# Kernel optimization log

Hardware: AMD Instinct MI355X
Metric: run time of the kernel (lower is better)

The kernel has to match this reference:

```python
import jax, jax.numpy as jnp
from jax import lax
import numpy as np


def setup_inputs() -> dict:
    key = jax.random.key(0)
    ks = jax.random.split(key, 9)
    B, T, F, E, H, O = 64, 512, 64, 256, 512, 128
    s = lambda k, shape, fan: jax.random.normal(k, shape, jnp.float32) / np.sqrt(fan)
    return {
        "x": jax.random.normal(ks[0], (B, T, F), jnp.float32),
        "W_emb": s(ks[1], (E, F), F),
        "b_emb": jnp.zeros((E,), jnp.float32),
        "W_ih": s(ks[2], (4 * H, E), E),
        "W_hh": s(ks[3], (4 * H, H), H),
        "b_ih": jnp.zeros((4 * H,), jnp.float32),
        "b_hh": jnp.zeros((4 * H,), jnp.float32),
        "W_fc": s(ks[4], (O, H), H),
        "b_fc": jnp.zeros((O,), jnp.float32),
    }


def reference(x, W_emb, b_emb, W_ih, W_hh, b_ih, b_hh, W_fc, b_fc):
    # Linear embedding: [B,T,F] -> [B,T,E]
    e = jnp.einsum("btf,ef->bte", x, W_emb) + b_emb
    # Precompute input-side gate projections once (big GEMM): [B,T,4H]
    xg = jnp.einsum("bte,ge->btg", e, W_ih) + b_ih + b_hh
    B = x.shape[0]
    H = W_hh.shape[1]
    W_hh_T = W_hh.T  # [H,4H]

    def step(carry, xt):
        h, c = carry
        gates = xt + h @ W_hh_T  # [B,4H]
        i, f, g, o = jnp.split(gates, 4, axis=-1)  # PyTorch LSTM gate order
        i = jax.nn.sigmoid(i)
        f = jax.nn.sigmoid(f)
        g = jnp.tanh(g)
        o = jax.nn.sigmoid(o)
        c = f * c + i * g
        h = o * jnp.tanh(c)
        return (h, c), h

    h0 = jnp.zeros((B, H), x.dtype)
    _, hs = lax.scan(step, (h0, h0), jnp.swapaxes(xg, 0, 1))  # hs: [T,B,H]
    # AdaptiveAvgPool1d(1) over time -> mean over T
    pooled = hs.mean(axis=0)  # [B,H]
    return pooled @ W_fc.T + b_fc  # [B,O]
```

## Files before the change

### kernel.cpp

```cpp
#include <hip/hip_runtime.h>
#include <math.h>

#define TS 512
#define NB 64
#define NF 64
#define NE 256
#define NH 512
#define NO 128

#define NGRP 4
#define NSLC 32
#define RPG  16

#define OFF_WCOMB 0
#define OFF_BCOMB 131072
#define OFF_HBUF  133120
#define OFF_POOL  198656

typedef short bf16x8 __attribute__((ext_vector_type(8)));
typedef float f32x4 __attribute__((ext_vector_type(4)));
typedef unsigned long long u64;
typedef unsigned int u32;

union F8 { bf16x8 s; unsigned short u[8]; };

__device__ __forceinline__ unsigned short f2bf(float f) {
    unsigned u = __float_as_uint(f);
    u += 0x7fffu + ((u >> 16) & 1u);
    return (unsigned short)(u >> 16);
}
__device__ __forceinline__ float bf2f(unsigned short h) {
    return __uint_as_float(((unsigned)h) << 16);
}
__device__ __forceinline__ float fast_sigmoid(float v) {
    return 1.f / (1.f + __expf(-v));
}
__device__ __forceinline__ float fast_tanh(float v) {
    return 1.f - 2.f / (1.f + __expf(2.f * v));
}
__device__ __forceinline__ u32 aload(const u32* p) {
    return __hip_atomic_load(p, __ATOMIC_RELAXED, __HIP_MEMORY_SCOPE_AGENT);
}

__global__ __launch_bounds__(256) void k_wcomb(const float* __restrict__ W_emb,
                                               const float* __restrict__ b_emb,
                                               const float* __restrict__ W_ih,
                                               const float* __restrict__ b_ih,
                                               const float* __restrict__ b_hh,
                                               float* __restrict__ W_comb,
                                               float* __restrict__ b_comb) {
    __shared__ float wih[4][NE];
    int g0 = blockIdx.x * 4;
    for (int i = threadIdx.x; i < 4 * NE; i += 256)
        wih[i >> 8][i & 255] = W_ih[(size_t)g0 * NE + i];
    __syncthreads();
    int gl = threadIdx.x >> 6, f = threadIdx.x & 63;
    float acc = 0.f;
    for (int e = 0; e < NE; ++e) acc += wih[gl][e] * W_emb[e * NF + f];
    W_comb[(size_t)(g0 + gl) * NF + f] = acc;
    if (f == 0) {
        float a2 = 0.f;
        for (int e = 0; e < NE; ++e) a2 += wih[gl][e] * b_emb[e];
        b_comb[g0 + gl] = a2 + b_ih[g0 + gl] + b_hh[g0 + gl];
    }
}

__global__ __launch_bounds__(512, 1) void k_lstm(const float* __restrict__ x,
                                                 const float* __restrict__ W_hh,
                                                 const float* __restrict__ W_comb,
                                                 const float* __restrict__ b_comb,
                                                 u32* __restrict__ hbuf,
                                                 float* __restrict__ pooled) {
    const int wg = blockIdx.x;
    const int grp = wg & 3;
    const int slc = wg >> 2;
    const int tid = threadIdx.x;
    const int lane = tid & 63, wave = tid >> 6;
    const int m4 = lane & 15;
    const int qq = lane >> 4;

    const int mtn = (wave < 6) ? 2 : 3;
    int kts[3];
    kts[0] = (wave < 6) ? 2 * wave : 12 + 2 * (wave - 6);
    kts[1] = kts[0] + 1;
    kts[2] = (wave < 6) ? 0 : 16 + (wave - 6);

    __shared__ __align__(16) float part[8 * 64 * 20];
    __shared__ float bcl[64];

    F8 bhi[4][3], blo[4][3];
    #pragma unroll
    for (int nt = 0; nt < 4; ++nt) {
        const int grow = nt * NH + slc * 16 + m4;
        #pragma unroll
        for (int k = 0; k < 3; ++k) {
            if (k < mtn) {
                const int kt = kts[k];
                const float* wp = (kt < 16)
                    ? W_hh   + (size_t)grow * NH + kt * 32 + qq * 8
                    : W_comb + (size_t)grow * NF + (kt - 16) * 32 + qq * 8;
                const float4 w0 = *(const float4*)wp;
                const float4 w1 = *(const float4*)(wp + 4);
                float wf[8] = {w0.x, w0.y, w0.z, w0.w, w1.x, w1.y, w1.z, w1.w};
                #pragma unroll
                for (int e = 0; e < 8; ++e) {
                    unsigned short hb = f2bf(wf[e]);
                    bhi[nt][k].u[e] = hb;
                    blo[nt][k].u[e] = f2bf(wf[e] - bf2f(hb));
                }
            }
        }
    }

    if (tid < 64) bcl[tid] = b_comb[(tid >> 4) * NH + slc * 16 + (tid & 15)];

    F8 ahi[3], alo[3];
    #pragma unroll
    for (int k = 0; k < 3; ++k) {
        ahi[k].s = (bf16x8){0, 0, 0, 0, 0, 0, 0, 0};
        alo[k].s = (bf16x8){0, 0, 0, 0, 0, 0, 0, 0};
    }
    float4 xpa = make_float4(0.f, 0.f, 0.f, 0.f), xpb = xpa;
    if (wave >= 6) {
        const int xoff = (wave - 6) * 32 + qq * 8;
        const float* xr0 = x + ((size_t)(grp * RPG + m4) * TS + 0) * NF + xoff;
        const float4 a = ((const float4*)xr0)[0];
        const float4 b4 = ((const float4*)xr0)[1];
        float xf[8] = {a.x, a.y, a.z, a.w, b4.x, b4.y, b4.z, b4.w};
        #pragma unroll
        for (int e = 0; e < 8; ++e) {
            unsigned short hb = f2bf(xf[e]);
            ahi[2].u[e] = hb;
            alo[2].u[e] = f2bf(xf[e] - bf2f(hb));
        }
        const float* xr1 = x + ((size_t)(grp * RPG + m4) * TS + 1) * NF + xoff;
        xpa = ((const float4*)xr1)[0];
        xpb = ((const float4*)xr1)[1];
    }

    float c_reg = 0.f, hsum = 0.f;
    __syncthreads();

    for (int t = 0; t < TS; ++t) {
        const bool last = (t + 1 == TS);
        const int p = t & 1;

        f32x4 acc[4][3];
        #pragma unroll
        for (int nt = 0; nt < 4; ++nt)
            #pragma unroll
            for (int c = 0; c < 3; ++c) acc[nt][c] = (f32x4){0.f, 0.f, 0.f, 0.f};
        #pragma unroll
        for (int k = 0; k < 3; ++k) {
            if (k < mtn) {
                const bf16x8 ah = ahi[k].s;
                const bf16x8 al = alo[k].s;
                #pragma unroll
                for (int nt = 0; nt < 4; ++nt) {
                    acc[nt][0] = __builtin_amdgcn_mfma_f32_16x16x32_bf16(ah, bhi[nt][k].s, acc[nt][0], 0, 0, 0);
                    acc[nt][1] = __builtin_amdgcn_mfma_f32_16x16x32_bf16(al, bhi[nt][k].s, acc[nt][1], 0, 0, 0);
                    acc[nt][2] = __builtin_amdgcn_mfma_f32_16x16x32_bf16(ah, blo[nt][k].s, acc[nt][2], 0, 0, 0);
                }
            }
        }
        #pragma unroll
        for (int nt = 0; nt < 4; ++nt) {
            const f32x4 a = acc[nt][0] + acc[nt][1] + acc[nt][2];
            *(float4*)&part[wave * 1280 + (nt * 16 + m4) * 20 + qq * 4] =
                make_float4(a.x, a.y, a.z, a.w);
        }
        __syncthreads();

        const unsigned tg2 = (unsigned)(((t + 1) & 3) ^ 2);
        u32* const slab = hbuf + ((size_t)(p * NGRP + grp)) * 8192;

        if (tid < 256) {
            const int j = tid >> 4, b = tid & 15;
            float v[4];
            #pragma unroll
            for (int ty = 0; ty < 4; ++ty) {
                const int n_loc = ty * 16 + j;
                float s = bcl[n_loc];
                #pragma unroll
                for (int w = 0; w < 8; ++w) s += part[w * 1280 + n_loc * 20 + b];
                v[ty] = s;
            }
            const float iv = fast_sigmoid(v[0]);
            const float fv = fast_sigmoid(v[1]);
            const float gv = fast_tanh(v[2]);
            const float ov = fast_sigmoid(v[3]);
            c_reg = fv * c_reg + iv * gv;
            const float h = ov * fast_tanh(c_reg);
            hsum += h;
            if (!last) {
                const unsigned short hb = f2bf(h);
                const unsigned short lb = f2bf(h - bf2f(hb));
                const u32 pk = ((u32)hb << 16) | ((u32)lb & 0xFFFCu) | tg2;
                __hip_atomic_store(&slab[slc * 256 + tid], pk,
                                   __ATOMIC_RELAXED, __HIP_MEMORY_SCOPE_AGENT);
            }
        }
        __syncthreads();

        if (!last) {
            const u32* b0 = slab + (kts[0] * 4 + qq) * 128 + m4;
            const u32* b1 = slab + (kts[1] * 4 + qq) * 128 + m4;
            u32 wd[16];
            __builtin_amdgcn_s_sleep(8);
            #pragma unroll
            for (int j = 0; j < 8; ++j) wd[j] = aload(b0 + j * 16);
            #pragma unroll
            for (int j = 0; j < 8; ++j) wd[8 + j] = aload(b1 + j * 16);
            int guard = 0;
            for (;;) {
                u32 bad = 0;
                #pragma unroll
                for (int i = 0; i < 16; ++i) bad |= (wd[i] & 3) ^ tg2;
                if (bad == 0) break;
                if (guard < 16)      __builtin_amdgcn_s_sleep(1);
                else if (guard < 64) __builtin_amdgcn_s_sleep(2);
                else                 __builtin_amdgcn_s_sleep(4);
                #pragma unroll
                for (int j = 0; j < 8; ++j) wd[j] = aload(b0 + j * 16);
                #pragma unroll
                for (int j = 0; j < 8; ++j) wd[8 + j] = aload(b1 + j * 16);
                if (++guard > (1 << 20)) break;
            }
            #pragma unroll
            for (int j = 0; j < 8; ++j) {
                ahi[0].u[j] = (unsigned short)(wd[j] >> 16);
                alo[0].u[j] = (unsigned short)(wd[j] & 0xFFFCu);
                ahi[1].u[j] = (unsigned short)(wd[8 + j] >> 16);
                alo[1].u[j] = (unsigned short)(wd[8 + j] & 0xFFFCu);
            }
            if (wave >= 6) {
                const int xoff = (wave - 6) * 32 + qq * 8;
                float xf[8] = {xpa.x, xpa.y, xpa.z, xpa.w, xpb.x, xpb.y, xpb.z, xpb.w};
                #pragma unroll
                for (int e = 0; e < 8; ++e) {
                    unsigned short hb = f2bf(xf[e]);
                    ahi[2].u[e] = hb;
                    alo[2].u[e] = f2bf(xf[e] - bf2f(hb));
                }
                if (t + 2 < TS) {
                    const float* xr = x + ((size_t)(grp * RPG + m4) * TS + (t + 2)) * NF + xoff;
                    xpa = ((const float4*)xr)[0];
                    xpb = ((const float4*)xr)[1];
                }
            }
        }
    }

    if (tid < 256) {
        const int j = tid >> 4, b = tid & 15;
        pooled[(size_t)(grp * RPG + b) * NH + slc * 16 + j] = hsum * (1.f / TS);
    }
}

__global__ __launch_bounds__(256) void k_fc(const float* __restrict__ pooled,
                                            const float* __restrict__ W_fc,
                                            const float* __restrict__ b_fc,
                                            float* __restrict__ out) {
    __shared__ float pl[2][NH];
    const int b0 = blockIdx.x * 2;
    for (int i = threadIdx.x; i < 2 * NH; i += 256)
        pl[i >> 9][i & 511] = pooled[(size_t)b0 * NH + i];
    __syncthreads();
    const int o = threadIdx.x & 127, bl = threadIdx.x >> 7;
    const float* wr = W_fc + (size_t)o * NH;
    float acc = 0.f;
    #pragma unroll 4
    for (int k = 0; k < NH; k += 4) {
        const float4 wv = *(const float4*)&wr[k];
        acc += pl[bl][k] * wv.x + pl[bl][k + 1] * wv.y +
               pl[bl][k + 2] * wv.z + pl[bl][k + 3] * wv.w;
    }
    out[(size_t)(b0 + bl) * NO + o] = acc + b_fc[o];
}

extern "C" void kernel_launch(void* const* d_in, const int* in_sizes, int n_in,
                              void* d_out, int out_size, void* d_ws, size_t ws_size,
                              hipStream_t stream) {
    const float* x     = (const float*)d_in[0];
    const float* W_emb = (const float*)d_in[1];
    const float* b_emb = (const float*)d_in[2];
    const float* W_ih  = (const float*)d_in[3];
    const float* W_hh  = (const float*)d_in[4];
    const float* b_ih  = (const float*)d_in[5];
    const float* b_hh  = (const float*)d_in[6];
    const float* W_fc  = (const float*)d_in[7];
    const float* b_fc  = (const float*)d_in[8];
    float* out = (float*)d_out;
    float* ws  = (float*)d_ws;

    float* W_comb = ws + OFF_WCOMB;
    float* b_comb = ws + OFF_BCOMB;
    u32*   hbuf   = (u32*)(ws + OFF_HBUF);
    float* pooled = ws + OFF_POOL;

    hipLaunchKernelGGL(k_wcomb, dim3(512), dim3(256), 0, stream,
                       W_emb, b_emb, W_ih, b_ih, b_hh, W_comb, b_comb);
    hipLaunchKernelGGL(k_lstm,  dim3(128), dim3(512), 0, stream,
                       x, W_hh, W_comb, b_comb, hbuf, pooled);
    hipLaunchKernelGGL(k_fc,    dim3(32),  dim3(256), 0, stream,
                       pooled, W_fc, b_fc, out);
}
```

Before: 1.274 ms.

## Overlap recurrent MFMA with per-slab h polling in persistent LSTM loop

The recurrent matmul moves out of the top of each timestep and into the wait phase of the previous step. The two hidden-state slabs are now polled one after the other, and the MFMAs for the first slab run while the second slab is still arriving from other workgroups. The input-projection MFMAs for wave 6 and above are also issued as soon as the next x tile is converted, with one extra issue before the loop. This aims to hide the cross-workgroup exchange latency behind compute, at the cost of a second spin loop and accumulators that stay live across the step boundary.

```diff
diff --git a/kernel.cpp b/kernel.cpp
--- a/kernel.cpp
+++ b/kernel.cpp
@@ -138,6 +138,20 @@
         xpb = ((const float4*)xr1)[1];
     }
 
+    f32x4 acc[4][3];
+    #pragma unroll
+    for (int nt = 0; nt < 4; ++nt)
+        #pragma unroll
+        for (int c = 0; c < 3; ++c) acc[nt][c] = (f32x4){0.f, 0.f, 0.f, 0.f};
+    if (wave >= 6) {
+        #pragma unroll
+        for (int nt = 0; nt < 4; ++nt) {
+            acc[nt][0] = __builtin_amdgcn_mfma_f32_16x16x32_bf16(ahi[2].s, bhi[nt][2].s, acc[nt][0], 0, 0, 0);
+            acc[nt][1] = __builtin_amdgcn_mfma_f32_16x16x32_bf16(alo[2].s, bhi[nt][2].s, acc[nt][1], 0, 0, 0);
+            acc[nt][2] = __builtin_amdgcn_mfma_f32_16x16x32_bf16(ahi[2].s, blo[nt][2].s, acc[nt][2], 0, 0, 0);
+        }
+    }
+
     float c_reg = 0.f, hsum = 0.f;
     __syncthreads();
 
@@ -145,24 +159,6 @@
         const bool last = (t + 1 == TS);
         const int p = t & 1;
 
-        f32x4 acc[4][3];
-        #pragma unroll
-        for (int nt = 0; nt < 4; ++nt)
-            #pragma unroll
-            for (int c = 0; c < 3; ++c) acc[nt][c] = (f32x4){0.f, 0.f, 0.f, 0.f};
-        #pragma unroll
-        for (int k = 0; k < 3; ++k) {
-            if (k < mtn) {
-                const bf16x8 ah = ahi[k].s;
-                const bf16x8 al = alo[k].s;
-                #pragma unroll
-                for (int nt = 0; nt < 4; ++nt) {
-                    acc[nt][0] = __builtin_amdgcn_mfma_f32_16x16x32_bf16(ah, bhi[nt][k].s, acc[nt][0], 0, 0, 0);
-                    acc[nt][1] = __builtin_amdgcn_mfma_f32_16x16x32_bf16(al, bhi[nt][k].s, acc[nt][1], 0, 0, 0);
-                    acc[nt][2] = __builtin_amdgcn_mfma_f32_16x16x32_bf16(ah, blo[nt][k].s, acc[nt][2], 0, 0, 0);
-                }
-            }
-        }
         #pragma unroll
         for (int nt = 0; nt < 4; ++nt) {
             const f32x4 a = acc[nt][0] + acc[nt][1] + acc[nt][2];
@@ -205,34 +201,69 @@
         if (!last) {
             const u32* b0 = slab + (kts[0] * 4 + qq) * 128 + m4;
             const u32* b1 = slab + (kts[1] * 4 + qq) * 128 + m4;
-            u32 wd[16];
+            u32 wd[8];
+
+            #pragma unroll
+            for (int nt = 0; nt < 4; ++nt)
+                #pragma unroll
+                for (int c = 0; c < 3; ++c) acc[nt][c] = (f32x4){0.f, 0.f, 0.f, 0.f};
+
             __builtin_amdgcn_s_sleep(8);
+
             #pragma unroll
             for (int j = 0; j < 8; ++j) wd[j] = aload(b0 + j * 16);
-            #pragma unroll
-            for (int j = 0; j < 8; ++j) wd[8 + j] = aload(b1 + j * 16);
             int guard = 0;
             for (;;) {
                 u32 bad = 0;
                 #pragma unroll
-                for (int i = 0; i < 16; ++i) bad |= (wd[i] & 3) ^ tg2;
+                for (int i = 0; i < 8; ++i) bad |= (wd[i] & 3) ^ tg2;
                 if (bad == 0) break;
                 if (guard < 16)      __builtin_amdgcn_s_sleep(1);
                 else if (guard < 64) __builtin_amdgcn_s_sleep(2);
                 else                 __builtin_amdgcn_s_sleep(4);
                 #pragma unroll
                 for (int j = 0; j < 8; ++j) wd[j] = aload(b0 + j * 16);
-                #pragma unroll
-                for (int j = 0; j < 8; ++j) wd[8 + j] = aload(b1 + j * 16);
                 if (++guard > (1 << 20)) break;
             }
             #pragma unroll
             for (int j = 0; j < 8; ++j) {
                 ahi[0].u[j] = (unsigned short)(wd[j] >> 16);
                 alo[0].u[j] = (unsigned short)(wd[j] & 0xFFFCu);
-                ahi[1].u[j] = (unsigned short)(wd[8 + j] >> 16);
-                alo[1].u[j] = (unsigned short)(wd[8 + j] & 0xFFFCu);
-            }
+            }
+            #pragma unroll
+            for (int nt = 0; nt < 4; ++nt) {
+                acc[nt][0] = __builtin_amdgcn_mfma_f32_16x16x32_bf16(ahi[0].s, bhi[nt][0].s, acc[nt][0], 0, 0, 0);
+                acc[nt][1] = __builtin_amdgcn_mfma_f32_16x16x32_bf16(alo[0].s, bhi[nt][0].s, acc[nt][1], 0, 0, 0);
+                acc[nt][2] = __builtin_amdgcn_mfma_f32_16x16x32_bf16(ahi[0].s, blo[nt][0].s, acc[nt][2], 0, 0, 0);
+            }
+
+            #pragma unroll
+            for (int j = 0; j < 8; ++j) wd[j] = aload(b1 + j * 16);
+            guard = 0;
+            for (;;) {
+                u32 bad = 0;
+                #pragma unroll
+                for (int i = 0; i < 8; ++i) bad |= (wd[i] & 3) ^ tg2;
+                if (bad == 0) break;
+                if (guard < 16)      __builtin_amdgcn_s_sleep(1);
+                else if (guard < 64) __builtin_amdgcn_s_sleep(2);
+                else                 __builtin_amdgcn_s_sleep(4);
+                #pragma unroll
+                for (int j = 0; j < 8; ++j) wd[j] = aload(b1 + j * 16);
+                if (++guard > (1 << 20)) break;
+            }
+            #pragma unroll
+            for (int j = 0; j < 8; ++j) {
+                ahi[1].u[j] = (unsigned short)(wd[j] >> 16);
+                alo[1].u[j] = (unsigned short)(wd[j] & 0xFFFCu);
+            }
+            #pragma unroll
+            for (int nt = 0; nt < 4; ++nt) {
+                acc[nt][0] = __builtin_amdgcn_mfma_f32_16x16x32_bf16(ahi[1].s, bhi[nt][1].s, acc[nt][0], 0, 0, 0);
+                acc[nt][1] = __builtin_amdgcn_mfma_f32_16x16x32_bf16(alo[1].s, bhi[nt][1].s, acc[nt][1], 0, 0, 0);
+                acc[nt][2] = __builtin_amdgcn_mfma_f32_16x16x32_bf16(ahi[1].s, blo[nt][1].s, acc[nt][2], 0, 0, 0);
+            }
+
             if (wave >= 6) {
                 const int xoff = (wave - 6) * 32 + qq * 8;
                 float xf[8] = {xpa.x, xpa.y, xpa.z, xpa.w, xpb.x, xpb.y, xpb.z, xpb.w};
@@ -241,6 +272,12 @@
                     unsigned short hb = f2bf(xf[e]);
                     ahi[2].u[e] = hb;
                     alo[2].u[e] = f2bf(xf[e] - bf2f(hb));
+                }
+                #pragma unroll
+                for (int nt = 0; nt < 4; ++nt) {
+                    acc[nt][0] = __builtin_amdgcn_mfma_f32_16x16x32_bf16(ahi[2].s, bhi[nt][2].s, acc[nt][0], 0, 0, 0);
+                    acc[nt][1] = __builtin_amdgcn_mfma_f32_16x16x32_bf16(alo[2].s, bhi[nt][2].s, acc[nt][1], 0, 0, 0);
+                    acc[nt][2] = __builtin_amdgcn_mfma_f32_16x16x32_bf16(ahi[2].s, blo[nt][2].s, acc[nt][2], 0, 0, 0);
                 }
                 if (t + 2 < TS) {
                     const float* xr = x + ((size_t)(grp * RPG + m4) * TS + (t + 2)) * NF + xoff;
```

Result: no change. 1.260 ms (-1.1%).
